# Kernel optimization log

Measured on AMD Instinct MI355X. Metric: run time of the kernel, lower is better.

## Reference

```python
import jax, jax.numpy as jnp
import numpy as np

N_NODES = 100000
N_EDGES = 1600000
IN_D = 128
MID_D = 64
N_CLASSES = 40
NEG_SLOPE = 0.2


def setup_inputs() -> dict:
    key = jax.random.key(0)
    ks = jax.random.split(key, 12)
    x = jax.random.normal(ks[0], (N_NODES, IN_D), dtype=jnp.float32)
    edge_index = jax.random.randint(ks[1], (2, N_EDGES), 0, N_NODES, dtype=jnp.int64)
    s = 0.1
    return {
        "x": x,
        "edge_index": edge_index,
        "W0": jax.random.normal(ks[2], (IN_D, MID_D), dtype=jnp.float32) * s,
        "as0": jax.random.normal(ks[3], (MID_D,), dtype=jnp.float32) * s,
        "ad0": jax.random.normal(ks[4], (MID_D,), dtype=jnp.float32) * s,
        "b0": jnp.zeros((MID_D,), dtype=jnp.float32),
        "W1": jax.random.normal(ks[5], (MID_D, MID_D), dtype=jnp.float32) * s,
        "as1": jax.random.normal(ks[6], (MID_D,), dtype=jnp.float32) * s,
        "ad1": jax.random.normal(ks[7], (MID_D,), dtype=jnp.float32) * s,
        "b1": jnp.zeros((MID_D,), dtype=jnp.float32),
        "Wc": jax.random.normal(ks[8], (MID_D, N_CLASSES), dtype=jnp.float32) * s,
        "bc": jnp.zeros((N_CLASSES,), dtype=jnp.float32),
    }


def gat_conv(x, src, dst, W, a_src, a_dst, b):
    """Single-head PyG GATConv (self-loops already appended to src/dst)."""
    n = x.shape[0]
    h = x @ W                                  # [N, d]
    e = jax.nn.leaky_relu((h @ a_src)[src] + (h @ a_dst)[dst], NEG_SLOPE)  # [E]
    # segment softmax over incoming edges of each destination node
    emax = jax.ops.segment_max(e, dst, num_segments=n)
    ee = jnp.exp(e - emax[dst])
    denom = jax.ops.segment_sum(ee, dst, num_segments=n)
    alpha = ee / (denom[dst] + 1e-16)          # [E]
    out = jax.ops.segment_sum(h[src] * alpha[:, None], dst, num_segments=n)
    return out + b


def reference(x, edge_index, W0, as0, ad0, b0, W1, as1, ad1, b1, Wc, bc):
    n = x.shape[0]
    loop = jnp.arange(n, dtype=edge_index.dtype)
    src = jnp.concatenate([edge_index[0], loop])
    dst = jnp.concatenate([edge_index[1], loop])
    h = jax.nn.relu(gat_conv(x, src, dst, W0, as0, ad0, b0))
    h = jax.nn.relu(gat_conv(h, src, dst, W1, as1, ad1, b1))
    logits = h @ Wc + bc
    return jax.nn.log_softmax(logits, axis=1)
```

## Files before the change

kernel.cpp:

```cpp
#include <hip/hip_runtime.h>
#include <hip/hip_bf16.h>
#include <math.h>

typedef __attribute__((ext_vector_type(8))) short bf16x8;
typedef __attribute__((ext_vector_type(4))) float f32x4;


__device__ __forceinline__ short f2bf(float f) {
    unsigned u = __float_as_uint(f);
    u += 0x7fff + ((u >> 16) & 1);
    return (short)(u >> 16);
}
__device__ __forceinline__ float bf2f(unsigned short s) {
    return __uint_as_float(((unsigned)s) << 16);
}

__device__ __forceinline__ int load_idx(const void* ei, long long pos, int is64) {
    if (is64) return (int)((const long long*)ei)[pos];
    return ((const int*)ei)[pos];
}


#define TILE 4096
#define NBKT_MAX 512
#define CAP 12288

__global__ __launch_bounds__(1024) void csr_init(
        const unsigned* __restrict__ ei, int* __restrict__ flag,
        int* __restrict__ gCursor) {
    int tid = threadIdx.x;
    if (tid < NBKT_MAX) gCursor[tid] = 0;
    if (tid == 0) {
        int ok = (ei[1] == 0u) & (ei[3] == 0u) & (ei[5] == 0u) &
                 (ei[7] == 0u) & (ei[9] == 0u) & (ei[11] == 0u);
        *flag = ok;
    }
}

__global__ __launch_bounds__(256) void prep_weights(
        const float* __restrict__ W0, const float* __restrict__ W1,
        const float* __restrict__ Wc,
        unsigned short* __restrict__ W0t, unsigned short* __restrict__ W1t,
        unsigned short* __restrict__ Wct) {
    int t = (int)(blockIdx.x * (size_t)blockDim.x + threadIdx.x);
    int stride = (int)(gridDim.x * (size_t)blockDim.x);
    for (int i = t; i < 64 * 128; i += stride) {
        int col = i >> 7, k = i & 127;
        W0t[i] = (unsigned short)f2bf(W0[k * 64 + col]);
    }
    for (int i = t; i < 64 * 64; i += stride) {
        int col = i >> 6, k = i & 63;
        W1t[i] = (unsigned short)f2bf(W1[k * 64 + col]);
    }
    for (int i = t; i < 48 * 64; i += stride) {
        int col = i >> 6, k = i & 63;
        Wct[i] = (col < 40) ? (unsigned short)f2bf(Wc[k * 40 + col]) : 0;
    }
}

__global__ __launch_bounds__(1024) void bucket_scatter(
        const void* __restrict__ ei, const int* __restrict__ flag,
        int* __restrict__ gCursor, unsigned* __restrict__ packed, int E, int N) {
    __shared__ int h[NBKT_MAX], excl[NBKT_MAX], bse[NBKT_MAX], cur[NBKT_MAX];
    __shared__ unsigned pck[TILE];
    __shared__ int tgt[TILE];
    int tid = threadIdx.x;
    int is64 = *flag;
    int total = E + N;
    int base = blockIdx.x * TILE;

    if (tid < NBKT_MAX) h[tid] = 0;
    __syncthreads();

    int s[4], d[4];
    bool ok[4];
#pragma unroll
    for (int j = 0; j < 4; j++) {
        int t = base + j * 1024 + tid;
        ok[j] = t < total;
        if (ok[j]) {
            if (t < E) { s[j] = load_idx(ei, t, is64); d[j] = load_idx(ei, (long long)E + t, is64); }
            else       { s[j] = d[j] = t - E; }
            atomicAdd(&h[d[j] >> 8], 1);
        }
    }
    __syncthreads();
    if (tid < NBKT_MAX) excl[tid] = h[tid];
    __syncthreads();
    for (int off = 1; off < NBKT_MAX; off <<= 1) {
        int v = (tid < NBKT_MAX && tid >= off) ? excl[tid - off] : 0;
        __syncthreads();
        if (tid < NBKT_MAX) excl[tid] += v;
        __syncthreads();
    }
    if (tid < NBKT_MAX) {
        excl[tid] -= h[tid];
        cur[tid] = excl[tid];
        bse[tid] = h[tid] ? atomicAdd(gCursor + tid, h[tid]) : 0;
    }
    __syncthreads();
#pragma unroll
    for (int j = 0; j < 4; j++) {
        if (ok[j]) {
            int b = d[j] >> 8;
            int ls = atomicAdd(&cur[b], 1);
            pck[ls] = ((unsigned)(d[j] & 255) << 17) | (unsigned)s[j];
            int off = bse[b] + (ls - excl[b]);
            tgt[ls] = (off < CAP) ? (b * CAP + off) : -1;
        }
    }
    __syncthreads();
    int nvalid = total - base; if (nvalid > TILE) nvalid = TILE;
    for (int i = tid; i < nvalid; i += 1024)
        if (tgt[i] >= 0) packed[tgt[i]] = pck[i];
}

__global__ __launch_bounds__(512) void bucket_scan(
        const int* __restrict__ gCursor, int* __restrict__ bucketStart) {
    __shared__ int sb[NBKT_MAX];
    int tid = threadIdx.x;
    int c = gCursor[tid];
    sb[tid] = c > CAP ? CAP : c;
    __syncthreads();
    for (int off = 1; off < NBKT_MAX; off <<= 1) {
        int v = (tid >= off) ? sb[tid - off] : 0;
        __syncthreads();
        sb[tid] += v;
        __syncthreads();
    }
    bucketStart[tid + 1] = sb[tid];
    if (tid == 0) bucketStart[0] = 0;
}

__global__ __launch_bounds__(1024) void bucket_finalize(
        const int* __restrict__ gCursor, const int* __restrict__ bucketStart,
        const unsigned* __restrict__ packed,
        int* __restrict__ rowptr, int* __restrict__ srcs, int N, int TOT) {
    __shared__ unsigned arr2[CAP];
    __shared__ int cnt2[256], sc[256], cur[256];
    int tid = threadIdx.x;
    int b = blockIdx.x;
    int bs = bucketStart[b];
    int cnt = gCursor[b]; if (cnt > CAP) cnt = CAP;
    int nNodes = N - b * 256; if (nNodes > 256) nNodes = 256;

    if (tid < 256) cnt2[tid] = 0;
    __syncthreads();

    unsigned pv[12];
#pragma unroll
    for (int i = 0; i < 12; i++) {
        int idx = i * 1024 + tid;
        if (idx < cnt) pv[i] = packed[(size_t)b * CAP + idx];
    }
#pragma unroll
    for (int i = 0; i < 12; i++) {
        int idx = i * 1024 + tid;
        if (idx < cnt) atomicAdd(&cnt2[pv[i] >> 17], 1);
    }
    __syncthreads();
    if (tid < 256) sc[tid] = cnt2[tid];
    __syncthreads();
    for (int off = 1; off < 256; off <<= 1) {
        int v = (tid < 256 && tid >= off) ? sc[tid - off] : 0;
        __syncthreads();
        if (tid < 256) sc[tid] += v;
        __syncthreads();
    }
    if (tid < 256) cur[tid] = sc[tid] - cnt2[tid];
    if (tid < nNodes) rowptr[b * 256 + tid] = bs + sc[tid] - cnt2[tid];
    if (b == 0 && tid == 0) rowptr[N] = TOT;
    __syncthreads();

#pragma unroll
    for (int i = 0; i < 12; i++) {
        int idx = i * 1024 + tid;
        if (idx < cnt) {
            int pos = atomicAdd(&cur[pv[i] >> 17], 1);
            arr2[pos] = pv[i] & 0x1FFFFu;
        }
    }
    __syncthreads();

    int wid = tid >> 6, lane = tid & 63;
    int half = lane >> 5, hl = lane & 31;
    for (int n2 = wid * 2; n2 < nNodes; n2 += 32) {
        int n = n2 + half;
        int deg = (n < nNodes) ? cnt2[n] : 0;
        if (deg >= 1 && deg <= 32) {
            int segs = sc[n] - deg;
            int v = (hl < deg) ? (int)arr2[segs + hl] : 0x7fffffff;
#pragma unroll
            for (int k = 2; k <= 32; k <<= 1) {
#pragma unroll
                for (int j = 16; j > 0; j >>= 1) {
                    if (j < k) {
                        int other = __shfl_xor(v, j);
                        bool dirDesc = (hl & k) != 0;
                        bool lower = (hl & j) == 0;
                        bool takeMin = (lower != dirDesc);
                        int mn = v < other ? v : other;
                        int mx = v < other ? other : v;
                        v = takeMin ? mn : mx;
                    }
                }
            }
            if (hl < deg) srcs[bs + segs + hl] = v;
        }
    }
    for (int n = wid; n < nNodes; n += 16) {
        int deg = cnt2[n];
        if (deg <= 32) continue;
        int segs = sc[n] - deg;
        if (deg <= 64) {
            int v = (lane < deg) ? (int)arr2[segs + lane] : 0x7fffffff;
#pragma unroll
            for (int k = 2; k <= 64; k <<= 1) {
#pragma unroll
                for (int j = 32; j > 0; j >>= 1) {
                    if (j < k) {
                        int other = __shfl_xor(v, j);
                        bool dirDesc = (lane & k) != 0;
                        bool lower = (lane & j) == 0;
                        bool takeMin = (lower != dirDesc);
                        int mn = v < other ? v : other;
                        int mx = v < other ? other : v;
                        v = takeMin ? mn : mx;
                    }
                }
            }
            if (lane < deg) srcs[bs + segs + lane] = v;
        } else if (lane == 0) {
            for (int i = segs + 1; i < segs + deg; i++) {
                unsigned key = arr2[i];
                int j = i - 1;
                while (j >= segs && arr2[j] > key) { arr2[j + 1] = arr2[j]; j--; }
                arr2[j + 1] = key;
            }
            for (int i = 0; i < deg; i++) srcs[bs + segs + i] = (int)arr2[segs + i];
        }
    }
}

template <int K, typename XT>
__global__ __launch_bounds__(256) void gemm_mfma(
        const XT* __restrict__ X, const unsigned short* __restrict__ Wt,
        const float* __restrict__ a_s, const float* __restrict__ a_d,
        unsigned short* __restrict__ Hbf,
        float* __restrict__ Sv, float* __restrict__ Dv, int N) {
    constexpr int KS = K / 32;
    int wid = threadIdx.x >> 6;
    int lane = threadIdx.x & 63;
    int base = blockIdx.x * 64 + wid * 16;
    if (base >= N) return;
    int l15 = lane & 15, lhi = lane >> 4;

    bf16x8 bfrag[KS][4];
#pragma unroll
    for (int ct = 0; ct < 4; ct++) {
        const unsigned short* wcol = Wt + (size_t)(ct * 16 + l15) * K + lhi * 8;
#pragma unroll
        for (int ks = 0; ks < KS; ks++)
            bfrag[ks][ct] = *(const bf16x8*)(wcol + ks * 32);
    }

    int row = base + l15; if (row >= N) row = N - 1;
    const XT* xr = X + (size_t)row * K + lhi * 8;
    bf16x8 afrag[KS];
#pragma unroll
    for (int ks = 0; ks < KS; ks++) {
        if constexpr (sizeof(XT) == 4) {
            float4 u0 = *(const float4*)(xr + ks * 32);
            float4 u1 = *(const float4*)(xr + ks * 32 + 4);
            afrag[ks][0] = f2bf(u0.x); afrag[ks][1] = f2bf(u0.y);
            afrag[ks][2] = f2bf(u0.z); afrag[ks][3] = f2bf(u0.w);
            afrag[ks][4] = f2bf(u1.x); afrag[ks][5] = f2bf(u1.y);
            afrag[ks][6] = f2bf(u1.z); afrag[ks][7] = f2bf(u1.w);
        } else {
            afrag[ks] = *(const bf16x8*)(xr + ks * 32);
        }
    }

    f32x4 acc[4] = {{0.f,0.f,0.f,0.f},{0.f,0.f,0.f,0.f},{0.f,0.f,0.f,0.f},{0.f,0.f,0.f,0.f}};
#pragma unroll
    for (int ks = 0; ks < KS; ks++)
#pragma unroll
        for (int ct = 0; ct < 4; ct++)
            acc[ct] = __builtin_amdgcn_mfma_f32_16x16x32_bf16(afrag[ks], bfrag[ks][ct], acc[ct], 0, 0, 0);

    float asv[4], adv[4];
#pragma unroll
    for (int ct = 0; ct < 4; ct++) { asv[ct] = a_s[ct * 16 + l15]; adv[ct] = a_d[ct * 16 + l15]; }

#pragma unroll
    for (int r = 0; r < 4; r++) {
        int grow = base + lhi * 4 + r;
        bool ok = grow < N;
        float sv = 0.f, dv = 0.f;
#pragma unroll
        for (int ct = 0; ct < 4; ct++) {
            float v = acc[ct][r];
            if (ok) Hbf[(size_t)grow * 64 + ct * 16 + l15] = (unsigned short)f2bf(v);
            sv = fmaf(v, asv[ct], sv);
            dv = fmaf(v, adv[ct], dv);
        }
#pragma unroll
        for (int off = 1; off < 16; off <<= 1) {
            sv += __shfl_xor(sv, off);
            dv += __shfl_xor(dv, off);
        }
        if (ok && l15 == 0) { Sv[grow] = sv; Dv[grow] = dv; }
    }
}

__global__ __launch_bounds__(256) void gat_agg_q(
        const int* __restrict__ rowptr, const int* __restrict__ srcs,
        const unsigned short* __restrict__ H, const float* __restrict__ Sv,
        const float* __restrict__ Dv, const float* __restrict__ b,
        unsigned short* __restrict__ OutRow, int N) {
    int wv = (int)((blockIdx.x * (size_t)blockDim.x + threadIdx.x) >> 6);
    int lane = threadIdx.x & 63;
    int q = lane >> 4, ql = lane & 15;
    int node = wv * 4 + q;
    if (node >= N) return;
    int start = rowptr[node];
    int deg = rowptr[node + 1] - start;
    float dvv = Dv[node];

    const uint2* Hd = (const uint2*)H;
    float a0 = 0.f, a1 = 0.f, a2 = 0.f, a3 = 0.f, den = 0.f;

    int sN0 = 0, sN1 = 0, sN2 = 0, sN3 = 0;
    if (deg >= 4) {
        sN0 = srcs[start];     sN1 = srcs[start + 1];
        sN2 = srcs[start + 2]; sN3 = srcs[start + 3];
    }
    int j = 0;
    for (; j + 4 <= deg; j += 4) {
        int s0 = sN0, s1 = sN1, s2 = sN2, s3 = sN3;
        if (j + 8 <= deg) {
            sN0 = srcs[start + j + 4]; sN1 = srcs[start + j + 5];
            sN2 = srcs[start + j + 6]; sN3 = srcs[start + j + 7];
        }
        float e0 = Sv[s0] + dvv, e1 = Sv[s1] + dvv,
              e2 = Sv[s2] + dvv, e3 = Sv[s3] + dvv;
        uint2 h0 = Hd[(size_t)s0 * 16 + ql];
        uint2 h1 = Hd[(size_t)s1 * 16 + ql];
        uint2 h2 = Hd[(size_t)s2 * 16 + ql];
        uint2 h3 = Hd[(size_t)s3 * 16 + ql];
        e0 = (e0 > 0.f) ? e0 : 0.2f * e0;
        e1 = (e1 > 0.f) ? e1 : 0.2f * e1;
        e2 = (e2 > 0.f) ? e2 : 0.2f * e2;
        e3 = (e3 > 0.f) ? e3 : 0.2f * e3;
        float p0 = __expf(e0), p1 = __expf(e1), p2 = __expf(e2), p3 = __expf(e3);
        den += (p0 + p1) + (p2 + p3);
        a0 = fmaf(p0, __uint_as_float(h0.x << 16), a0);
        a1 = fmaf(p0, __uint_as_float(h0.x & 0xffff0000u), a1);
        a2 = fmaf(p0, __uint_as_float(h0.y << 16), a2);
        a3 = fmaf(p0, __uint_as_float(h0.y & 0xffff0000u), a3);
        a0 = fmaf(p1, __uint_as_float(h1.x << 16), a0);
        a1 = fmaf(p1, __uint_as_float(h1.x & 0xffff0000u), a1);
        a2 = fmaf(p1, __uint_as_float(h1.y << 16), a2);
        a3 = fmaf(p1, __uint_as_float(h1.y & 0xffff0000u), a3);
        a0 = fmaf(p2, __uint_as_float(h2.x << 16), a0);
        a1 = fmaf(p2, __uint_as_float(h2.x & 0xffff0000u), a1);
        a2 = fmaf(p2, __uint_as_float(h2.y << 16), a2);
        a3 = fmaf(p2, __uint_as_float(h2.y & 0xffff0000u), a3);
        a0 = fmaf(p3, __uint_as_float(h3.x << 16), a0);
        a1 = fmaf(p3, __uint_as_float(h3.x & 0xffff0000u), a1);
        a2 = fmaf(p3, __uint_as_float(h3.y << 16), a2);
        a3 = fmaf(p3, __uint_as_float(h3.y & 0xffff0000u), a3);
    }
    for (; j < deg; j++) {
        int s0 = srcs[start + j];
        float e0 = Sv[s0] + dvv;
        uint2 h0 = Hd[(size_t)s0 * 16 + ql];
        e0 = (e0 > 0.f) ? e0 : 0.2f * e0;
        float p0 = __expf(e0);
        den += p0;
        a0 = fmaf(p0, __uint_as_float(h0.x << 16), a0);
        a1 = fmaf(p0, __uint_as_float(h0.x & 0xffff0000u), a1);
        a2 = fmaf(p0, __uint_as_float(h0.y << 16), a2);
        a3 = fmaf(p0, __uint_as_float(h0.y & 0xffff0000u), a3);
    }

    float rden = 1.0f / (den + 1e-16f);
    float4 bb = *(const float4*)(b + ql * 4);
    float v0 = fmaf(a0, rden, bb.x); v0 = v0 > 0.f ? v0 : 0.f;
    float v1 = fmaf(a1, rden, bb.y); v1 = v1 > 0.f ? v1 : 0.f;
    float v2 = fmaf(a2, rden, bb.z); v2 = v2 > 0.f ? v2 : 0.f;
    float v3 = fmaf(a3, rden, bb.w); v3 = v3 > 0.f ? v3 : 0.f;
    uint2 pack;
    pack.x = ((unsigned)(unsigned short)f2bf(v1) << 16) | (unsigned short)f2bf(v0);
    pack.y = ((unsigned)(unsigned short)f2bf(v3) << 16) | (unsigned short)f2bf(v2);
    *(uint2*)(OutRow + (size_t)node * 64 + ql * 4) = pack;
}

__global__ __launch_bounds__(256) void classifier_mfma(
        const unsigned short* __restrict__ H, const unsigned short* __restrict__ Wct,
        const float* __restrict__ bc, float* __restrict__ out, int N) {
    int wid = threadIdx.x >> 6;
    int lane = threadIdx.x & 63;
    int base = blockIdx.x * 64 + wid * 16;
    if (base >= N) return;
    int l15 = lane & 15, lhi = lane >> 4;
    int colv[3]; bool cok[3];
#pragma unroll
    for (int ct = 0; ct < 3; ct++) { colv[ct] = ct * 16 + l15; cok[ct] = colv[ct] < 40; }

    bf16x8 bfrag[2][3];
#pragma unroll
    for (int ct = 0; ct < 3; ct++) {
        const unsigned short* wcol = Wct + (size_t)colv[ct] * 64 + lhi * 8;
#pragma unroll
        for (int ks = 0; ks < 2; ks++)
            bfrag[ks][ct] = *(const bf16x8*)(wcol + ks * 32);
    }

    int row = base + l15; if (row >= N) row = N - 1;
    const unsigned short* xr = H + (size_t)row * 64 + lhi * 8;
    bf16x8 afrag[2] = { *(const bf16x8*)xr, *(const bf16x8*)(xr + 32) };

    f32x4 acc[3] = {{0.f,0.f,0.f,0.f},{0.f,0.f,0.f,0.f},{0.f,0.f,0.f,0.f}};
#pragma unroll
    for (int ks = 0; ks < 2; ks++)
#pragma unroll
        for (int ct = 0; ct < 3; ct++)
            acc[ct] = __builtin_amdgcn_mfma_f32_16x16x32_bf16(afrag[ks], bfrag[ks][ct], acc[ct], 0, 0, 0);

    float bcv[3];
#pragma unroll
    for (int ct = 0; ct < 3; ct++) bcv[ct] = cok[ct] ? bc[colv[ct]] : 0.f;

#pragma unroll
    for (int r = 0; r < 4; r++) {
        int node = base + lhi * 4 + r;
        bool ok = node < N;
        float lg[3];
#pragma unroll
        for (int ct = 0; ct < 3; ct++)
            lg[ct] = cok[ct] ? (acc[ct][r] + bcv[ct]) : -INFINITY;
        float m = fmaxf(fmaxf(lg[0], lg[1]), lg[2]);
#pragma unroll
        for (int off = 1; off < 16; off <<= 1) m = fmaxf(m, __shfl_xor(m, off));
        float ex = 0.f;
#pragma unroll
        for (int ct = 0; ct < 3; ct++) ex += cok[ct] ? __expf(lg[ct] - m) : 0.f;
#pragma unroll
        for (int off = 1; off < 16; off <<= 1) ex += __shfl_xor(ex, off);
        float ls = __logf(ex);
        if (ok) {
#pragma unroll
            for (int ct = 0; ct < 3; ct++)
                if (cok[ct]) out[(size_t)node * 40 + colv[ct]] = lg[ct] - m - ls;
        }
    }
}


extern "C" void kernel_launch(void* const* d_in, const int* in_sizes, int n_in,
                              void* d_out, int out_size, void* d_ws, size_t ws_size,
                              hipStream_t stream) {
    const float* x   = (const float*)d_in[0];
    const void*  ei  = d_in[1];
    const float* W0  = (const float*)d_in[2];
    const float* as0 = (const float*)d_in[3];
    const float* ad0 = (const float*)d_in[4];
    const float* b0  = (const float*)d_in[5];
    const float* W1  = (const float*)d_in[6];
    const float* as1 = (const float*)d_in[7];
    const float* ad1 = (const float*)d_in[8];
    const float* b1  = (const float*)d_in[9];
    const float* Wc  = (const float*)d_in[10];
    const float* bc  = (const float*)d_in[11];
    float* out = (float*)d_out;

    const int N = in_sizes[0] / 128;
    const int E = in_sizes[1] / 2;
    const int TOT = E + N;
    const int nbkt = (N + 255) / 256;

    char* w = (char*)d_ws;
    unsigned short* HAbf    = (unsigned short*)w; w += (size_t)N * 64 * 2;
    unsigned short* HCbf    = (unsigned short*)w; w += (size_t)N * 64 * 2;
    float*          Sv      = (float*)w;          w += (size_t)N * 4;
    float*          Dv      = (float*)w;          w += (size_t)N * 4;
    int*            rowptr  = (int*)w;            w += (size_t)(N + 1) * 4;
    int*            srcs    = (int*)w;            w += (size_t)TOT * 4;
    unsigned*       packed  = (unsigned*)w;       w += (size_t)nbkt * CAP * 4;
    int*            gCursor = (int*)w;            w += NBKT_MAX * 4;
    int*            bktStart= (int*)w;            w += (NBKT_MAX + 1) * 4;
    int*            flag    = (int*)w;            w += 256;
    unsigned short* W0t     = (unsigned short*)w; w += 64 * 128 * 2;
    unsigned short* W1t     = (unsigned short*)w; w += 64 * 64 * 2;
    unsigned short* Wct     = (unsigned short*)w; w += 48 * 64 * 2;

    const int B = 256;
    const int gQuad  = (N + 15) / 16;
    const int gTile  = (N + 63) / 64;
    const int nTileE = (TOT + TILE - 1) / TILE;

    csr_init<<<1, 1024, 0, stream>>>((const unsigned*)ei, flag, gCursor);
    prep_weights<<<8, B, 0, stream>>>(W0, W1, Wc, W0t, W1t, Wct);
    bucket_scatter<<<nTileE, 1024, 0, stream>>>(ei, flag, gCursor, packed, E, N);
    bucket_scan<<<1, NBKT_MAX, 0, stream>>>(gCursor, bktStart);
    bucket_finalize<<<nbkt, 1024, 0, stream>>>(gCursor, bktStart, packed, rowptr, srcs, N, TOT);

    gemm_mfma<128, float><<<gTile, B, 0, stream>>>(x, W0t, as0, ad0, HAbf, Sv, Dv, N);
    gat_agg_q<<<gQuad, B, 0, stream>>>(rowptr, srcs, HAbf, Sv, Dv, b0, HCbf, N);

    gemm_mfma<64, unsigned short><<<gTile, B, 0, stream>>>(HCbf, W1t, as1, ad1, HAbf, Sv, Dv, N);
    gat_agg_q<<<gQuad, B, 0, stream>>>(rowptr, srcs, HAbf, Sv, Dv, b1, HCbf, N);

    classifier_mfma<<<gTile, B, 0, stream>>>(HCbf, Wct, bc, out, N);
}
```

Before: 179.4 us.

## Shrink CSR buckets to 128 nodes and fold init and bucket scan into neighbors

Merges the cursor/flag init kernel into the weight-prep kernel, and removes the separate bucket-scan kernel by having each finalize block reduce the preceding bucket counts itself. Buckets shrink from 256 to 128 destination nodes, with smaller per-bucket capacity and 512-thread finalize blocks, which gives more, lighter blocks. The aggregation kernel drops its software prefetch of the next four source indices in favour of direct loads. Trade-offs: fewer launches and better occupancy in finalize, but redundant prefix sums per block, a tighter overflow cap, and possibly more exposed load latency in the aggregation loop.

```diff
diff --git a/kernel.cpp b/kernel.cpp
--- a/kernel.cpp
+++ b/kernel.cpp
@@ -22,28 +22,25 @@
 
 
 #define TILE 4096
-#define NBKT_MAX 512
-#define CAP 12288
-
-__global__ __launch_bounds__(1024) void csr_init(
+#define NBKT_MAX 1024
+#define BKT_SH 7
+#define CAP 6912
+
+__global__ __launch_bounds__(256) void prep_init(
         const unsigned* __restrict__ ei, int* __restrict__ flag,
-        int* __restrict__ gCursor) {
-    int tid = threadIdx.x;
-    if (tid < NBKT_MAX) gCursor[tid] = 0;
-    if (tid == 0) {
-        int ok = (ei[1] == 0u) & (ei[3] == 0u) & (ei[5] == 0u) &
-                 (ei[7] == 0u) & (ei[9] == 0u) & (ei[11] == 0u);
-        *flag = ok;
-    }
-}
-
-__global__ __launch_bounds__(256) void prep_weights(
+        int* __restrict__ gCursor,
         const float* __restrict__ W0, const float* __restrict__ W1,
         const float* __restrict__ Wc,
         unsigned short* __restrict__ W0t, unsigned short* __restrict__ W1t,
         unsigned short* __restrict__ Wct) {
     int t = (int)(blockIdx.x * (size_t)blockDim.x + threadIdx.x);
     int stride = (int)(gridDim.x * (size_t)blockDim.x);
+    for (int i = t; i < NBKT_MAX; i += stride) gCursor[i] = 0;
+    if (t == 0) {
+        int ok = (ei[1] == 0u) & (ei[3] == 0u) & (ei[5] == 0u) &
+                 (ei[7] == 0u) & (ei[9] == 0u) & (ei[11] == 0u);
+        *flag = ok;
+    }
     for (int i = t; i < 64 * 128; i += stride) {
         int col = i >> 7, k = i & 127;
         W0t[i] = (unsigned short)f2bf(W0[k * 64 + col]);
@@ -69,7 +66,7 @@
     int total = E + N;
     int base = blockIdx.x * TILE;
 
-    if (tid < NBKT_MAX) h[tid] = 0;
+    h[tid] = 0;
     __syncthreads();
 
     int s[4], d[4];
@@ -81,30 +78,28 @@
         if (ok[j]) {
             if (t < E) { s[j] = load_idx(ei, t, is64); d[j] = load_idx(ei, (long long)E + t, is64); }
             else       { s[j] = d[j] = t - E; }
-            atomicAdd(&h[d[j] >> 8], 1);
-        }
-    }
-    __syncthreads();
-    if (tid < NBKT_MAX) excl[tid] = h[tid];
+            atomicAdd(&h[d[j] >> BKT_SH], 1);
+        }
+    }
+    __syncthreads();
+    excl[tid] = h[tid];
     __syncthreads();
     for (int off = 1; off < NBKT_MAX; off <<= 1) {
-        int v = (tid < NBKT_MAX && tid >= off) ? excl[tid - off] : 0;
+        int v = (tid >= off) ? excl[tid - off] : 0;
         __syncthreads();
-        if (tid < NBKT_MAX) excl[tid] += v;
+        excl[tid] += v;
         __syncthreads();
     }
-    if (tid < NBKT_MAX) {
-        excl[tid] -= h[tid];
-        cur[tid] = excl[tid];
-        bse[tid] = h[tid] ? atomicAdd(gCursor + tid, h[tid]) : 0;
-    }
+    excl[tid] -= h[tid];
+    cur[tid] = excl[tid];
+    bse[tid] = h[tid] ? atomicAdd(gCursor + tid, h[tid]) : 0;
     __syncthreads();
 #pragma unroll
     for (int j = 0; j < 4; j++) {
         if (ok[j]) {
-            int b = d[j] >> 8;
+            int b = d[j] >> BKT_SH;
             int ls = atomicAdd(&cur[b], 1);
-            pck[ls] = ((unsigned)(d[j] & 255) << 17) | (unsigned)s[j];
+            pck[ls] = ((unsigned)(d[j] & 127) << 17) | (unsigned)s[j];
             int off = bse[b] + (ls - excl[b]);
             tgt[ls] = (off < CAP) ? (b * CAP + off) : -1;
         }
@@ -115,66 +110,61 @@
         if (tgt[i] >= 0) packed[tgt[i]] = pck[i];
 }
 
-__global__ __launch_bounds__(512) void bucket_scan(
-        const int* __restrict__ gCursor, int* __restrict__ bucketStart) {
-    __shared__ int sb[NBKT_MAX];
-    int tid = threadIdx.x;
-    int c = gCursor[tid];
-    sb[tid] = c > CAP ? CAP : c;
-    __syncthreads();
-    for (int off = 1; off < NBKT_MAX; off <<= 1) {
-        int v = (tid >= off) ? sb[tid - off] : 0;
-        __syncthreads();
-        sb[tid] += v;
-        __syncthreads();
-    }
-    bucketStart[tid + 1] = sb[tid];
-    if (tid == 0) bucketStart[0] = 0;
-}
-
-__global__ __launch_bounds__(1024) void bucket_finalize(
-        const int* __restrict__ gCursor, const int* __restrict__ bucketStart,
-        const unsigned* __restrict__ packed,
+__global__ __launch_bounds__(512) void bucket_finalize(
+        const int* __restrict__ gCursor, const unsigned* __restrict__ packed,
         int* __restrict__ rowptr, int* __restrict__ srcs, int N, int TOT) {
     __shared__ unsigned arr2[CAP];
-    __shared__ int cnt2[256], sc[256], cur[256];
+    __shared__ int cnt2[128], sc[128], cur[128];
+    __shared__ int red[512];
     int tid = threadIdx.x;
     int b = blockIdx.x;
-    int bs = bucketStart[b];
+
+    int accs = 0;
+    for (int i = tid; i < b; i += 512) {
+        int c = gCursor[i];
+        accs += (c > CAP ? CAP : c);
+    }
+    red[tid] = accs;
+    __syncthreads();
+    for (int off = 256; off > 0; off >>= 1) {
+        if (tid < off) red[tid] += red[tid + off];
+        __syncthreads();
+    }
+    int bs = red[0];
     int cnt = gCursor[b]; if (cnt > CAP) cnt = CAP;
-    int nNodes = N - b * 256; if (nNodes > 256) nNodes = 256;
-
-    if (tid < 256) cnt2[tid] = 0;
-    __syncthreads();
-
-    unsigned pv[12];
-#pragma unroll
-    for (int i = 0; i < 12; i++) {
-        int idx = i * 1024 + tid;
+    int nNodes = N - (b << BKT_SH); if (nNodes > 128) nNodes = 128;
+
+    if (tid < 128) cnt2[tid] = 0;
+    __syncthreads();
+
+    unsigned pv[14];
+#pragma unroll
+    for (int i = 0; i < 14; i++) {
+        int idx = i * 512 + tid;
         if (idx < cnt) pv[i] = packed[(size_t)b * CAP + idx];
     }
 #pragma unroll
-    for (int i = 0; i < 12; i++) {
-        int idx = i * 1024 + tid;
+    for (int i = 0; i < 14; i++) {
+        int idx = i * 512 + tid;
         if (idx < cnt) atomicAdd(&cnt2[pv[i] >> 17], 1);
     }
     __syncthreads();
-    if (tid < 256) sc[tid] = cnt2[tid];
-    __syncthreads();
-    for (int off = 1; off < 256; off <<= 1) {
-        int v = (tid < 256 && tid >= off) ? sc[tid - off] : 0;
+    if (tid < 128) sc[tid] = cnt2[tid];
+    __syncthreads();
+    for (int off = 1; off < 128; off <<= 1) {
+        int v = (tid < 128 && tid >= off) ? sc[tid - off] : 0;
         __syncthreads();
-        if (tid < 256) sc[tid] += v;
+        if (tid < 128) sc[tid] += v;
         __syncthreads();
     }
-    if (tid < 256) cur[tid] = sc[tid] - cnt2[tid];
-    if (tid < nNodes) rowptr[b * 256 + tid] = bs + sc[tid] - cnt2[tid];
+    if (tid < 128) cur[tid] = sc[tid] - cnt2[tid];
+    if (tid < nNodes) rowptr[(b << BKT_SH) + tid] = bs + sc[tid] - cnt2[tid];
     if (b == 0 && tid == 0) rowptr[N] = TOT;
     __syncthreads();
 
 #pragma unroll
-    for (int i = 0; i < 12; i++) {
-        int idx = i * 1024 + tid;
+    for (int i = 0; i < 14; i++) {
+        int idx = i * 512 + tid;
         if (idx < cnt) {
             int pos = atomicAdd(&cur[pv[i] >> 17], 1);
             arr2[pos] = pv[i] & 0x1FFFFu;
@@ -184,7 +174,7 @@
 
     int wid = tid >> 6, lane = tid & 63;
     int half = lane >> 5, hl = lane & 31;
-    for (int n2 = wid * 2; n2 < nNodes; n2 += 32) {
+    for (int n2 = wid * 2; n2 < nNodes; n2 += 16) {
         int n = n2 + half;
         int deg = (n < nNodes) ? cnt2[n] : 0;
         if (deg >= 1 && deg <= 32) {
@@ -208,7 +198,7 @@
             if (hl < deg) srcs[bs + segs + hl] = v;
         }
     }
-    for (int n = wid; n < nNodes; n += 16) {
+    for (int n = wid; n < nNodes; n += 8) {
         int deg = cnt2[n];
         if (deg <= 32) continue;
         int segs = sc[n] - deg;
@@ -330,18 +320,10 @@
     const uint2* Hd = (const uint2*)H;
     float a0 = 0.f, a1 = 0.f, a2 = 0.f, a3 = 0.f, den = 0.f;
 
-    int sN0 = 0, sN1 = 0, sN2 = 0, sN3 = 0;
-    if (deg >= 4) {
-        sN0 = srcs[start];     sN1 = srcs[start + 1];
-        sN2 = srcs[start + 2]; sN3 = srcs[start + 3];
-    }
     int j = 0;
     for (; j + 4 <= deg; j += 4) {
-        int s0 = sN0, s1 = sN1, s2 = sN2, s3 = sN3;
-        if (j + 8 <= deg) {
-            sN0 = srcs[start + j + 4]; sN1 = srcs[start + j + 5];
-            sN2 = srcs[start + j + 6]; sN3 = srcs[start + j + 7];
-        }
+        int s0 = srcs[start + j], s1 = srcs[start + j + 1],
+            s2 = srcs[start + j + 2], s3 = srcs[start + j + 3];
         float e0 = Sv[s0] + dvv, e1 = Sv[s1] + dvv,
               e2 = Sv[s2] + dvv, e3 = Sv[s3] + dvv;
         uint2 h0 = Hd[(size_t)s0 * 16 + ql];
@@ -478,7 +460,7 @@
     const int N = in_sizes[0] / 128;
     const int E = in_sizes[1] / 2;
     const int TOT = E + N;
-    const int nbkt = (N + 255) / 256;
+    const int nbkt = (N + 127) / 128;
 
     char* w = (char*)d_ws;
     unsigned short* HAbf    = (unsigned short*)w; w += (size_t)N * 64 * 2;
@@ -489,7 +471,6 @@
     int*            srcs    = (int*)w;            w += (size_t)TOT * 4;
     unsigned*       packed  = (unsigned*)w;       w += (size_t)nbkt * CAP * 4;
     int*            gCursor = (int*)w;            w += NBKT_MAX * 4;
-    int*            bktStart= (int*)w;            w += (NBKT_MAX + 1) * 4;
     int*            flag    = (int*)w;            w += 256;
     unsigned short* W0t     = (unsigned short*)w; w += 64 * 128 * 2;
     unsigned short* W1t     = (unsigned short*)w; w += 64 * 64 * 2;
@@ -500,11 +481,10 @@
     const int gTile  = (N + 63) / 64;
     const int nTileE = (TOT + TILE - 1) / TILE;
 
-    csr_init<<<1, 1024, 0, stream>>>((const unsigned*)ei, flag, gCursor);
-    prep_weights<<<8, B, 0, stream>>>(W0, W1, Wc, W0t, W1t, Wct);
+    prep_init<<<8, B, 0, stream>>>((const unsigned*)ei, flag, gCursor,
+                                   W0, W1, Wc, W0t, W1t, Wct);
     bucket_scatter<<<nTileE, 1024, 0, stream>>>(ei, flag, gCursor, packed, E, N);
-    bucket_scan<<<1, NBKT_MAX, 0, stream>>>(gCursor, bktStart);
-    bucket_finalize<<<nbkt, 1024, 0, stream>>>(gCursor, bktStart, packed, rowptr, srcs, N, TOT);
+    bucket_finalize<<<nbkt, 512, 0, stream>>>(gCursor, packed, rowptr, srcs, N, TOT);
 
     gemm_mfma<128, float><<<gTile, B, 0, stream>>>(x, W0t, as0, ad0, HAbf, Sv, Dv, N);
     gat_agg_q<<<gQuad, B, 0, stream>>>(rowptr, srcs, HAbf, Sv, Dv, b0, HCbf, N);
```

Measured after the change: 177.1 us. No clear change (-1.3%).
